# Kernel tuning notes

Hardware: AMD Instinct MI355X
Metric: run time of the kernel (lower is better)

The kernel has to match this reference:

```python
import jax, jax.numpy as jnp
import numpy as np

B, D, P, E = 256, 512, 128, 128  # batch, in_dim, nproto, projection_dim

def setup_inputs() -> dict:
    key = jax.random.key(0)
    k1, k2 = jax.random.split(key)
    x = jax.random.normal(k1, (B, D, P), dtype=jnp.float32)
    # glorot-uniform-like weights, one [D,E] matrix per prototype
    limit = jnp.sqrt(6.0 / (D + E)).astype(jnp.float32)
    W = jax.random.uniform(k2, (P, D, E), dtype=jnp.float32, minval=-limit, maxval=limit)
    b = jnp.zeros((P, E), dtype=jnp.float32)  # bias per prototype
    return {"x": x, "W": W, "b": b}

def reference(x, W, b):
    # Original: for each proto p, x[:,:,p] @ W_p + b_p, stacked on axis=2.
    # Fused as a single batched GEMM over the prototype axis.
    # x: [B,D,P], W: [P,D,E] -> out: [B,E,P]
    out = jnp.einsum('bdp,pde->bep', x, W)
    out = out + b.T[None, :, :]  # b: [P,E] -> broadcast [1,E,P]
    return out
```

## Files before the change

kernel.cpp:

```cpp
#include <hip/hip_runtime.h>
#include <cstdint>
#include <cstddef>

#define B_ 256
#define D_ 512
#define P_ 128
#define E_ 128

typedef unsigned short u16;
typedef unsigned int   u32;
typedef __bf16  bf16x8_t __attribute__((ext_vector_type(8)));
typedef float   f32x4_t  __attribute__((ext_vector_type(4)));
typedef u16     u16x4_t  __attribute__((ext_vector_type(4)));
typedef u16     u16x8_t  __attribute__((ext_vector_type(8)));

__device__ __forceinline__ u16 f2bf(float f) {
  union { float f; unsigned int u; } c; c.f = f;
  unsigned int u = c.u;
  unsigned int r = (u + 0x7FFFu + ((u >> 16) & 1u)) >> 16;
  return (u16)r;
}
__device__ __forceinline__ float bf2f(u16 v) {
  union { unsigned int u; float f; } c; c.u = (unsigned int)v << 16;
  return c.f;
}

__global__ __launch_bounds__(256) void transpose_both_kernel(
    const float* __restrict__ x, const float* __restrict__ W,
    u16* __restrict__ xT, u16* __restrict__ Wt) {
  __shared__ float tile[64][65];

  const int ob = blockIdx.x;
  const bool isX = (ob < B_);
  const int o = isX ? ob : (ob - B_);
  const float* src = isX ? x : W;
  u16* dst = isX ? xT : Wt;
  const size_t rs = isX ? (size_t)B_ * D_ : (size_t)D_;
  const size_t os = isX ? (size_t)D_ : (size_t)E_ * D_;

  const int r0 = blockIdx.y * 64;
  const int c0 = blockIdx.z * 64;
  const int t  = threadIdx.x;

  const float* s = src + (size_t)o * D_ * 128 + (size_t)r0 * 128 + c0;

  {
    const int lr = t >> 4;
    const int lc = (t & 15) * 4;
    #pragma unroll
    for (int it = 0; it < 4; ++it) {
      const int r = lr + it * 16;
      const float4 v = *reinterpret_cast<const float4*>(s + (size_t)r * 128 + lc);
      tile[r][lc + 0] = v.x; tile[r][lc + 1] = v.y;
      tile[r][lc + 2] = v.z; tile[r][lc + 3] = v.w;
    }
  }
  __syncthreads();

  {
    const int wc = t >> 3;
    const int wd = (t & 7) * 8;
    #pragma unroll
    for (int it = 0; it < 2; ++it) {
      const int c = wc + it * 32;
      u16x8_t pkv;
      #pragma unroll
      for (int j = 0; j < 8; ++j) pkv[j] = f2bf(tile[wd + j][c]);
      *reinterpret_cast<u16x8_t*>(dst + (size_t)(c0 + c) * rs +
                                  (size_t)o * os + r0 + wd) = pkv;
    }
  }
}


#define SWZ_ELEM(row, g) (((row) << 6) + ((((g) ^ ((row) & 7))) << 3))

__global__ __launch_bounds__(256, 3) void gemm_kernel(
    const u16* __restrict__ xT, const u16* __restrict__ Wt,
    const float* __restrict__ bias, u16* __restrict__ ws2) {
  __shared__ __attribute__((aligned(16))) u16 As[3][64 * 64];
  __shared__ __attribute__((aligned(16))) u16 Bs[3][64 * 64];

  const int wg   = blockIdx.x;
  const int xcd  = wg & 7;
  const int i    = wg >> 3;
  const int p    = xcd * 16 + (i & 15);
  const int tile = i >> 4;
  const int b0   = (tile & 3) * 64;
  const int e0t  = (tile >> 2) * 64;

  const int t    = threadIdx.x;
  const int lane = t & 63;
  const int wv   = t >> 6;
  const int wr   = wv >> 1;
  const int wc   = wv & 1;

  const u16* Ag = xT + (size_t)p * (B_ * D_) + (size_t)b0 * D_;
  const u16* Bg = Wt + ((size_t)p * E_ + e0t) * D_;

  const int r1 = t >> 3;
  const int sw = (((t & 7) ^ (r1 & 7)) << 3);

  const int fr = lane & 15;
  const int fq = lane >> 4;

  f32x4_t acc[2][2] = {};

#define STAGE_AB(buf, d0) do { \
    __builtin_amdgcn_global_load_lds( \
        (const __attribute__((address_space(1))) void*)(Ag + (size_t)r1 * D_ + (d0) + sw), \
        (__attribute__((address_space(3))) void*)&As[buf][wv * 512], 16, 0, 0); \
    __builtin_amdgcn_global_load_lds( \
        (const __attribute__((address_space(1))) void*)(Ag + (size_t)(r1 + 32) * D_ + (d0) + sw), \
        (__attribute__((address_space(3))) void*)&As[buf][2048 + wv * 512], 16, 0, 0); \
    __builtin_amdgcn_global_load_lds( \
        (const __attribute__((address_space(1))) void*)(Bg + (size_t)r1 * D_ + (d0) + sw), \
        (__attribute__((address_space(3))) void*)&Bs[buf][wv * 512], 16, 0, 0); \
    __builtin_amdgcn_global_load_lds( \
        (const __attribute__((address_space(1))) void*)(Bg + (size_t)(r1 + 32) * D_ + (d0) + sw), \
        (__attribute__((address_space(3))) void*)&Bs[buf][2048 + wv * 512], 16, 0, 0); \
  } while (0)

#define MFMA(a, b, c) __builtin_amdgcn_mfma_f32_16x16x32_bf16((a), (b), (c), 0, 0, 0)

#define K_ITER(KT, BUF, PREFETCH, VMSTR, LAST) do { \
    const int rowa = wr * 32 + fr, rowb = wc * 32 + fr; \
    bf16x8_t af0 = *reinterpret_cast<const bf16x8_t*>(&As[BUF][SWZ_ELEM(rowa, fq)]); \
    bf16x8_t af1 = *reinterpret_cast<const bf16x8_t*>(&As[BUF][SWZ_ELEM(rowa, 4 + fq)]); \
    bf16x8_t af2 = *reinterpret_cast<const bf16x8_t*>(&As[BUF][SWZ_ELEM(rowa + 16, fq)]); \
    bf16x8_t af3 = *reinterpret_cast<const bf16x8_t*>(&As[BUF][SWZ_ELEM(rowa + 16, 4 + fq)]); \
    bf16x8_t bf0 = *reinterpret_cast<const bf16x8_t*>(&Bs[BUF][SWZ_ELEM(rowb, fq)]); \
    bf16x8_t bf1 = *reinterpret_cast<const bf16x8_t*>(&Bs[BUF][SWZ_ELEM(rowb, 4 + fq)]); \
    bf16x8_t bf2 = *reinterpret_cast<const bf16x8_t*>(&Bs[BUF][SWZ_ELEM(rowb + 16, fq)]); \
    bf16x8_t bf3 = *reinterpret_cast<const bf16x8_t*>(&Bs[BUF][SWZ_ELEM(rowb + 16, 4 + fq)]); \
    asm volatile("s_waitcnt lgkmcnt(0)" ::: "memory"); \
    __builtin_amdgcn_sched_barrier(0); \
    __builtin_amdgcn_s_barrier(); \
    if (PREFETCH) STAGE_AB(BUF, ((KT) + 3) * 64); \
    acc[0][0] = MFMA(af0, bf0, acc[0][0]); \
    acc[0][1] = MFMA(af0, bf2, acc[0][1]); \
    acc[1][0] = MFMA(af2, bf0, acc[1][0]); \
    acc[1][1] = MFMA(af2, bf2, acc[1][1]); \
    acc[0][0] = MFMA(af1, bf1, acc[0][0]); \
    acc[0][1] = MFMA(af1, bf3, acc[0][1]); \
    acc[1][0] = MFMA(af3, bf1, acc[1][0]); \
    acc[1][1] = MFMA(af3, bf3, acc[1][1]); \
    if (!(LAST)) { \
      asm volatile("s_waitcnt " VMSTR ::: "memory"); \
      __builtin_amdgcn_sched_barrier(0); \
      __builtin_amdgcn_s_barrier(); \
    } \
  } while (0)

  STAGE_AB(0, 0);
  STAGE_AB(1, 64);
  STAGE_AB(2, 128);
  asm volatile("s_waitcnt vmcnt(8)" ::: "memory");
  __builtin_amdgcn_sched_barrier(0);
  __builtin_amdgcn_s_barrier();

  K_ITER(0, 0, 1, "vmcnt(8)", 0);
  K_ITER(1, 1, 1, "vmcnt(8)", 0);
  K_ITER(2, 2, 1, "vmcnt(8)", 0);
  K_ITER(3, 0, 1, "vmcnt(8)", 0);
  K_ITER(4, 1, 1, "vmcnt(8)", 0);
  K_ITER(5, 2, 0, "vmcnt(4)", 0);
  K_ITER(6, 0, 0, "vmcnt(0)", 0);
  K_ITER(7, 1, 0, "vmcnt(0)", 1);

#undef K_ITER
#undef MFMA
#undef STAGE_AB

  const int q4 = fq * 4;
  #pragma unroll
  for (int jj = 0; jj < 2; ++jj) {
    const int e  = e0t + wc * 32 + jj * 16 + fr;
    const float bv = bias[p * E_ + e];
    #pragma unroll
    for (int ii = 0; ii < 2; ++ii) {
      const int r0 = b0 + wr * 32 + ii * 16 + q4;
      #pragma unroll
      for (int rg = 0; rg < 4; ++rg) {
        ws2[((size_t)p * B_ + (r0 + rg)) * E_ + e] = f2bf(acc[ii][jj][rg] + bv);
      }
    }
  }
}

__global__ __launch_bounds__(256) void out_transpose_kernel(
    const u16* __restrict__ ws2, float* __restrict__ out) {
  __shared__ float tile[64][65];

  const int b  = blockIdx.x;
  const int p0 = blockIdx.y * 64;
  const int e0 = blockIdx.z * 64;
  const int t  = threadIdx.x;

  const u16* s = ws2 + ((size_t)p0 * B_ + b) * E_ + e0;

  {
    const int lr = t >> 4;
    const int lc = (t & 15) * 4;
    #pragma unroll
    for (int it = 0; it < 4; ++it) {
      const int r = lr + it * 16;
      const u16x4_t v = *reinterpret_cast<const u16x4_t*>(s + (size_t)r * (B_ * E_) + lc);
      tile[r][lc + 0] = bf2f(v[0]); tile[r][lc + 1] = bf2f(v[1]);
      tile[r][lc + 2] = bf2f(v[2]); tile[r][lc + 3] = bf2f(v[3]);
    }
  }
  __syncthreads();

  {
    const int c  = t >> 4;
    const int wd = (t & 15) * 4;
    #pragma unroll
    for (int it = 0; it < 4; ++it) {
      const int cc = c + it * 16;
      float4 v;
      v.x = tile[wd + 0][cc]; v.y = tile[wd + 1][cc];
      v.z = tile[wd + 2][cc]; v.w = tile[wd + 3][cc];
      *reinterpret_cast<float4*>(out + ((size_t)b * E_ + e0 + cc) * P_ + p0 + wd) = v;
    }
  }
}

__global__ __launch_bounds__(256) void naive_kernel(
    const float* __restrict__ x, const float* __restrict__ W,
    const float* __restrict__ bias, float* __restrict__ out) {
  const size_t idx = (size_t)blockIdx.x * 256 + threadIdx.x;
  const int p = (int)(idx & 127);
  const int e = (int)((idx >> 7) & 127);
  const int b = (int)(idx >> 14);
  float acc = bias[p * E_ + e];
  const float* xp = x + (size_t)b * D_ * P_ + p;
  const float* wp = W + (size_t)p * D_ * E_ + e;
  for (int d = 0; d < D_; ++d) acc += xp[(size_t)d * P_] * wp[(size_t)d * E_];
  out[idx] = acc;
}

extern "C" void kernel_launch(void* const* d_in, const int* in_sizes, int n_in,
                              void* d_out, int out_size, void* d_ws, size_t ws_size,
                              hipStream_t stream) {
  (void)in_sizes; (void)n_in; (void)out_size;
  const float* x    = (const float*)d_in[0];
  const float* W    = (const float*)d_in[1];
  const float* bias = (const float*)d_in[2];
  float* out = (float*)d_out;

  const size_t xT_bytes  = (size_t)P_ * B_ * D_ * 2;
  const size_t Wt_bytes  = (size_t)P_ * E_ * D_ * 2;
  const size_t ws2_bytes = (size_t)P_ * B_ * E_ * 2;

  if (ws_size < xT_bytes + Wt_bytes + ws2_bytes) {
    naive_kernel<<<dim3((B_ * E_ * P_) / 256), 256, 0, stream>>>(x, W, bias, out);
    return;
  }

  u16* xT  = (u16*)d_ws;
  u16* Wt  = (u16*)((char*)d_ws + xT_bytes);
  u16* ws2 = (u16*)((char*)d_ws + xT_bytes + Wt_bytes);

  transpose_both_kernel<<<dim3(B_ + P_, 8, 2), 256, 0, stream>>>(x, W, xT, Wt);
  gemm_kernel<<<dim3(1024), 256, 0, stream>>>(xT, Wt, bias, ws2);
  out_transpose_kernel<<<dim3(B_, 2, 2), 256, 0, stream>>>(ws2, out);
}
```

Before: 47.75 us.

## Enlarge GEMM tile to 128x128 with 8 waves and restructure transpose kernel

Each GEMM workgroup now computes a 128x128 output tile with 512 threads and a 4x2 accumulator array per wave. This replaces 64x64 tiles with 256 threads, cutting redundant global and LDS traffic for the A and B operands. The input transpose/convert kernel is also reworked: each block now handles a 32-column by full-D strip instead of 64x64 tiles, so writes are long contiguous rows. The trade-off is only 256 GEMM workgroups, which may underfill the 256 CUs, plus higher LDS and register use per block.

```diff
diff --git a/kernel.cpp b/kernel.cpp
--- a/kernel.cpp
+++ b/kernel.cpp
@@ -25,49 +25,46 @@
   return c.f;
 }
 
-__global__ __launch_bounds__(256) void transpose_both_kernel(
+__global__ __launch_bounds__(256) void transpose_cvt2_kernel(
     const float* __restrict__ x, const float* __restrict__ W,
     u16* __restrict__ xT, u16* __restrict__ Wt) {
-  __shared__ float tile[64][65];
-
-  const int ob = blockIdx.x;
-  const bool isX = (ob < B_);
-  const int o = isX ? ob : (ob - B_);
+  __shared__ float tile[32][516];
+
+  const int bid  = blockIdx.x;
+  const bool isX = (bid < 1024);
+  const int o    = isX ? (bid >> 2) : ((bid - 1024) >> 2);
+  const int c0   = (bid & 3) * 32;
   const float* src = isX ? x : W;
   u16* dst = isX ? xT : Wt;
-  const size_t rs = isX ? (size_t)B_ * D_ : (size_t)D_;
-  const size_t os = isX ? (size_t)D_ : (size_t)E_ * D_;
-
-  const int r0 = blockIdx.y * 64;
-  const int c0 = blockIdx.z * 64;
-  const int t  = threadIdx.x;
-
-  const float* s = src + (size_t)o * D_ * 128 + (size_t)r0 * 128 + c0;
-
-  {
-    const int lr = t >> 4;
-    const int lc = (t & 15) * 4;
-    #pragma unroll
-    for (int it = 0; it < 4; ++it) {
-      const int r = lr + it * 16;
-      const float4 v = *reinterpret_cast<const float4*>(s + (size_t)r * 128 + lc);
-      tile[r][lc + 0] = v.x; tile[r][lc + 1] = v.y;
-      tile[r][lc + 2] = v.z; tile[r][lc + 3] = v.w;
+  const size_t rs = isX ? (size_t)(B_ * D_) : (size_t)D_;
+  const size_t os = isX ? (size_t)D_ : (size_t)(E_ * D_);
+
+  const int t = threadIdx.x;
+
+  {
+    const float* s = src + (size_t)o * (D_ * 128) + c0 + (t & 7) * 4;
+    const int cl = (t & 7) * 4;
+    #pragma unroll
+    for (int j = 0; j < 16; ++j) {
+      const int d = (t >> 3) + 32 * j;
+      const float4 v = *reinterpret_cast<const float4*>(s + (size_t)d * 128);
+      tile[cl + 0][d] = v.x; tile[cl + 1][d] = v.y;
+      tile[cl + 2][d] = v.z; tile[cl + 3][d] = v.w;
     }
   }
   __syncthreads();
 
   {
-    const int wc = t >> 3;
-    const int wd = (t & 7) * 8;
-    #pragma unroll
-    for (int it = 0; it < 2; ++it) {
-      const int c = wc + it * 32;
-      u16x8_t pkv;
+    const int c = t >> 3;
+    const int m = t & 7;
+    u16* drow = dst + (size_t)(c0 + c) * rs + (size_t)o * os;
+    #pragma unroll
+    for (int it = 0; it < 8; ++it) {
+      const int db = m * 8 + it * 64;
+      u16x8_t pk;
       #pragma unroll
-      for (int j = 0; j < 8; ++j) pkv[j] = f2bf(tile[wd + j][c]);
-      *reinterpret_cast<u16x8_t*>(dst + (size_t)(c0 + c) * rs +
-                                  (size_t)o * os + r0 + wd) = pkv;
+      for (int k = 0; k < 8; ++k) pk[k] = f2bf(tile[c][db + k]);
+      *reinterpret_cast<u16x8_t*>(drow + db) = pk;
     }
   }
 }
@@ -75,28 +72,26 @@
 
 #define SWZ_ELEM(row, g) (((row) << 6) + ((((g) ^ ((row) & 7))) << 3))
 
-__global__ __launch_bounds__(256, 3) void gemm_kernel(
+__global__ __launch_bounds__(512, 2) void gemm_kernel(
     const u16* __restrict__ xT, const u16* __restrict__ Wt,
     const float* __restrict__ bias, u16* __restrict__ ws2) {
-  __shared__ __attribute__((aligned(16))) u16 As[3][64 * 64];
-  __shared__ __attribute__((aligned(16))) u16 Bs[3][64 * 64];
-
-  const int wg   = blockIdx.x;
-  const int xcd  = wg & 7;
-  const int i    = wg >> 3;
-  const int p    = xcd * 16 + (i & 15);
-  const int tile = i >> 4;
-  const int b0   = (tile & 3) * 64;
-  const int e0t  = (tile >> 2) * 64;
+  __shared__ __attribute__((aligned(16))) u16 As[3][128 * 64];
+  __shared__ __attribute__((aligned(16))) u16 Bs[3][128 * 64];
+
+  const int wg  = blockIdx.x;
+  const int xcd = wg & 7;
+  const int i   = wg >> 3;
+  const int p   = xcd * 16 + (i & 15);
+  const int b0  = (i >> 4) * 128;
 
   const int t    = threadIdx.x;
   const int lane = t & 63;
   const int wv   = t >> 6;
-  const int wr   = wv >> 1;
-  const int wc   = wv & 1;
+  const int wr   = wv >> 2;
+  const int wc   = wv & 3;
 
   const u16* Ag = xT + (size_t)p * (B_ * D_) + (size_t)b0 * D_;
-  const u16* Bg = Wt + ((size_t)p * E_ + e0t) * D_;
+  const u16* Bg = Wt + (size_t)p * (E_ * D_);
 
   const int r1 = t >> 3;
   const int sw = (((t & 7) ^ (r1 & 7)) << 3);
@@ -104,47 +99,46 @@
   const int fr = lane & 15;
   const int fq = lane >> 4;
 
-  f32x4_t acc[2][2] = {};
+  f32x4_t acc[4][2] = {};
+
+#define GLOAD(gp, lp) __builtin_amdgcn_global_load_lds( \
+    (const __attribute__((address_space(1))) void*)(gp), \
+    (__attribute__((address_space(3))) void*)(lp), 16, 0, 0)
 
 #define STAGE_AB(buf, d0) do { \
-    __builtin_amdgcn_global_load_lds( \
-        (const __attribute__((address_space(1))) void*)(Ag + (size_t)r1 * D_ + (d0) + sw), \
-        (__attribute__((address_space(3))) void*)&As[buf][wv * 512], 16, 0, 0); \
-    __builtin_amdgcn_global_load_lds( \
-        (const __attribute__((address_space(1))) void*)(Ag + (size_t)(r1 + 32) * D_ + (d0) + sw), \
-        (__attribute__((address_space(3))) void*)&As[buf][2048 + wv * 512], 16, 0, 0); \
-    __builtin_amdgcn_global_load_lds( \
-        (const __attribute__((address_space(1))) void*)(Bg + (size_t)r1 * D_ + (d0) + sw), \
-        (__attribute__((address_space(3))) void*)&Bs[buf][wv * 512], 16, 0, 0); \
-    __builtin_amdgcn_global_load_lds( \
-        (const __attribute__((address_space(1))) void*)(Bg + (size_t)(r1 + 32) * D_ + (d0) + sw), \
-        (__attribute__((address_space(3))) void*)&Bs[buf][2048 + wv * 512], 16, 0, 0); \
+    GLOAD(Ag + (size_t)r1 * D_ + (d0) + sw,        &As[buf][wv * 512]); \
+    GLOAD(Ag + (size_t)(r1 + 64) * D_ + (d0) + sw, &As[buf][4096 + wv * 512]); \
+    GLOAD(Bg + (size_t)r1 * D_ + (d0) + sw,        &Bs[buf][wv * 512]); \
+    GLOAD(Bg + (size_t)(r1 + 64) * D_ + (d0) + sw, &Bs[buf][4096 + wv * 512]); \
   } while (0)
 
 #define MFMA(a, b, c) __builtin_amdgcn_mfma_f32_16x16x32_bf16((a), (b), (c), 0, 0, 0)
 
 #define K_ITER(KT, BUF, PREFETCH, VMSTR, LAST) do { \
-    const int rowa = wr * 32 + fr, rowb = wc * 32 + fr; \
-    bf16x8_t af0 = *reinterpret_cast<const bf16x8_t*>(&As[BUF][SWZ_ELEM(rowa, fq)]); \
-    bf16x8_t af1 = *reinterpret_cast<const bf16x8_t*>(&As[BUF][SWZ_ELEM(rowa, 4 + fq)]); \
-    bf16x8_t af2 = *reinterpret_cast<const bf16x8_t*>(&As[BUF][SWZ_ELEM(rowa + 16, fq)]); \
-    bf16x8_t af3 = *reinterpret_cast<const bf16x8_t*>(&As[BUF][SWZ_ELEM(rowa + 16, 4 + fq)]); \
-    bf16x8_t bf0 = *reinterpret_cast<const bf16x8_t*>(&Bs[BUF][SWZ_ELEM(rowb, fq)]); \
-    bf16x8_t bf1 = *reinterpret_cast<const bf16x8_t*>(&Bs[BUF][SWZ_ELEM(rowb, 4 + fq)]); \
-    bf16x8_t bf2 = *reinterpret_cast<const bf16x8_t*>(&Bs[BUF][SWZ_ELEM(rowb + 16, fq)]); \
-    bf16x8_t bf3 = *reinterpret_cast<const bf16x8_t*>(&Bs[BUF][SWZ_ELEM(rowb + 16, 4 + fq)]); \
+    bf16x8_t af[4][2], bfr[2][2]; \
+    _Pragma("unroll") \
+    for (int ii = 0; ii < 4; ++ii) { \
+      const int rowa = wr * 64 + ii * 16 + fr; \
+      af[ii][0] = *reinterpret_cast<const bf16x8_t*>(&As[BUF][SWZ_ELEM(rowa, fq)]); \
+      af[ii][1] = *reinterpret_cast<const bf16x8_t*>(&As[BUF][SWZ_ELEM(rowa, 4 + fq)]); \
+    } \
+    _Pragma("unroll") \
+    for (int jj = 0; jj < 2; ++jj) { \
+      const int rowb = wc * 32 + jj * 16 + fr; \
+      bfr[jj][0] = *reinterpret_cast<const bf16x8_t*>(&Bs[BUF][SWZ_ELEM(rowb, fq)]); \
+      bfr[jj][1] = *reinterpret_cast<const bf16x8_t*>(&Bs[BUF][SWZ_ELEM(rowb, 4 + fq)]); \
+    } \
     asm volatile("s_waitcnt lgkmcnt(0)" ::: "memory"); \
     __builtin_amdgcn_sched_barrier(0); \
     __builtin_amdgcn_s_barrier(); \
     if (PREFETCH) STAGE_AB(BUF, ((KT) + 3) * 64); \
-    acc[0][0] = MFMA(af0, bf0, acc[0][0]); \
-    acc[0][1] = MFMA(af0, bf2, acc[0][1]); \
-    acc[1][0] = MFMA(af2, bf0, acc[1][0]); \
-    acc[1][1] = MFMA(af2, bf2, acc[1][1]); \
-    acc[0][0] = MFMA(af1, bf1, acc[0][0]); \
-    acc[0][1] = MFMA(af1, bf3, acc[0][1]); \
-    acc[1][0] = MFMA(af3, bf1, acc[1][0]); \
-    acc[1][1] = MFMA(af3, bf3, acc[1][1]); \
+    _Pragma("unroll") \
+    for (int kh = 0; kh < 2; ++kh) \
+      _Pragma("unroll") \
+      for (int ii = 0; ii < 4; ++ii) \
+        _Pragma("unroll") \
+        for (int jj = 0; jj < 2; ++jj) \
+          acc[ii][jj] = MFMA(af[ii][kh], bfr[jj][kh], acc[ii][jj]); \
     if (!(LAST)) { \
       asm volatile("s_waitcnt " VMSTR ::: "memory"); \
       __builtin_amdgcn_sched_barrier(0); \
@@ -171,15 +165,16 @@
 #undef K_ITER
 #undef MFMA
 #undef STAGE_AB
+#undef GLOAD
 
   const int q4 = fq * 4;
   #pragma unroll
   for (int jj = 0; jj < 2; ++jj) {
-    const int e  = e0t + wc * 32 + jj * 16 + fr;
+    const int e  = wc * 32 + jj * 16 + fr;
     const float bv = bias[p * E_ + e];
     #pragma unroll
-    for (int ii = 0; ii < 2; ++ii) {
-      const int r0 = b0 + wr * 32 + ii * 16 + q4;
+    for (int ii = 0; ii < 4; ++ii) {
+      const int r0 = b0 + wr * 64 + ii * 16 + q4;
       #pragma unroll
       for (int rg = 0; rg < 4; ++rg) {
         ws2[((size_t)p * B_ + (r0 + rg)) * E_ + e] = f2bf(acc[ii][jj][rg] + bv);
@@ -262,7 +257,7 @@
   u16* Wt  = (u16*)((char*)d_ws + xT_bytes);
   u16* ws2 = (u16*)((char*)d_ws + xT_bytes + Wt_bytes);
 
-  transpose_both_kernel<<<dim3(B_ + P_, 8, 2), 256, 0, stream>>>(x, W, xT, Wt);
-  gemm_kernel<<<dim3(1024), 256, 0, stream>>>(xT, Wt, bias, ws2);
+  transpose_cvt2_kernel<<<dim3(1536), 256, 0, stream>>>(x, W, xT, Wt);
+  gemm_kernel<<<dim3(256), 512, 0, stream>>>(xT, Wt, bias, ws2);
   out_transpose_kernel<<<dim3(B_, 2, 2), 256, 0, stream>>>(ws2, out);
 }
```

Result: faster. 44.90 us (-6.0%).
